# Kernel optimization log

Measured on AMD Instinct MI355X. Metric: run time of the kernel, lower is better.

## Reference

```python
import jax, jax.numpy as jnp
import numpy as np

N_NODE = 50000
N_EDGE = 625000
FDIM = 128
HID = 128
EPS = 1e-5


def setup_inputs() -> dict:
    key = jax.random.key(0)
    ks = jax.random.split(key, 12)
    node_feature = jax.random.normal(ks[0], (N_NODE, FDIM), dtype=jnp.float32)
    edge_matrix = jax.random.randint(ks[1], (2, N_EDGE), 0, N_NODE, dtype=jnp.int32)
    edge_feature = jax.random.normal(ks[2], (N_EDGE, FDIM), dtype=jnp.float32)
    in_dim = FDIM + FDIM  # concat(node, aggregated edge)
    s1 = 1.0 / np.sqrt(in_dim)
    s2 = 1.0 / np.sqrt(HID)
    W1 = jax.random.uniform(ks[3], (in_dim, HID), jnp.float32, -s1, s1)
    b1 = jax.random.uniform(ks[4], (HID,), jnp.float32, -s1, s1)
    W2 = jax.random.uniform(ks[5], (HID, HID), jnp.float32, -s2, s2)
    b2 = jax.random.uniform(ks[6], (HID,), jnp.float32, -s2, s2)
    W3 = jax.random.uniform(ks[7], (HID, FDIM), jnp.float32, -s2, s2)
    b3 = jax.random.uniform(ks[8], (FDIM,), jnp.float32, -s2, s2)
    gamma = jnp.ones((FDIM,), jnp.float32)
    beta = jnp.zeros((FDIM,), jnp.float32)
    return {"node_feature": node_feature, "edge_matrix": edge_matrix,
            "edge_feature": edge_feature, "W1": W1, "b1": b1, "W2": W2,
            "b2": b2, "W3": W3, "b3": b3, "gamma": gamma, "beta": beta}


def reference(node_feature, edge_matrix, edge_feature, W1, b1, W2, b2, W3, b3, gamma, beta):
    # receiver_idx = edge_matrix.T[:, 1] with edge_matrix [2, N_edge] -> row 1
    receiver_idx = edge_matrix[1]
    # scatter_add over receiver: [N_node, fdim]
    agg = jax.ops.segment_sum(edge_feature, receiver_idx, num_segments=node_feature.shape[0])
    x = jnp.concatenate([node_feature, agg], axis=-1)  # [N_node, 2*fdim]
    h = jax.nn.relu(x @ W1 + b1)
    h = jax.nn.relu(h @ W2 + b2)
    h = h @ W3 + b3
    # LayerNorm over last dim (eps = 1e-5, torch default)
    mu = jnp.mean(h, axis=-1, keepdims=True)
    var = jnp.mean((h - mu) ** 2, axis=-1, keepdims=True)
    h = (h - mu) * jax.lax.rsqrt(var + EPS) * gamma + beta
    return h + node_feature
```

## Files before the change

kernel.cpp:

```cpp
#include <hip/hip_runtime.h>
#include <hip/hip_bf16.h>

#define N_NODE 50000
#define N_EDGE 625000
#define FDIM 128
#define NB_SCAN 196

typedef __bf16 bf16x8 __attribute__((ext_vector_type(8)));
typedef float floatx4 __attribute__((ext_vector_type(4)));

#define MT 64
#define XS_LD 264
#define W_LD 40
#define H_LD 136

__global__ __launch_bounds__(256) void hist_kernel(
    const int* __restrict__ recv, int* __restrict__ count, int* __restrict__ pos)
{
    int e = blockIdx.x * 256 + threadIdx.x;
    if (e < N_EDGE) pos[e] = atomicAdd(&count[recv[e]], 1);
}

__global__ __launch_bounds__(256) void scan1_kernel(
    const int* __restrict__ count, int* __restrict__ off, int* __restrict__ bsum)
{
    __shared__ int s[256];
    int t = threadIdx.x;
    int i = blockIdx.x * 256 + t;
    int v = (i < N_NODE) ? count[i] : 0;
    s[t] = v;
    __syncthreads();
    for (int d = 1; d < 256; d <<= 1) {
        int x = (t >= d) ? s[t - d] : 0;
        __syncthreads();
        s[t] += x;
        __syncthreads();
    }
    if (i < N_NODE) off[i] = s[t] - v;
    if (t == 255) bsum[blockIdx.x] = s[255];
}

__global__ __launch_bounds__(256) void scan2_kernel(
    int* __restrict__ off, const int* __restrict__ bsum)
{
    __shared__ int s[256];
    int t = threadIdx.x;
    int v = (t < NB_SCAN) ? bsum[t] : 0;
    s[t] = v;
    __syncthreads();
    for (int d = 1; d < 256; d <<= 1) {
        int x = (t >= d) ? s[t - d] : 0;
        __syncthreads();
        s[t] += x;
        __syncthreads();
    }
    int i = blockIdx.x * 256 + t;
    if (i < N_NODE) off[i] += s[blockIdx.x] - ((blockIdx.x < NB_SCAN) ? bsum[blockIdx.x] : 0);
    if (i == N_NODE) off[i] = N_EDGE;
}

__global__ __launch_bounds__(256) void fill_kernel(
    const int* __restrict__ recv, const int* __restrict__ pos,
    const int* __restrict__ off, int* __restrict__ eid)
{
    int e = blockIdx.x * 256 + threadIdx.x;
    if (e < N_EDGE) {
        int r = recv[e];
        eid[off[r] + pos[e]] = e;
    }
}

__global__ __launch_bounds__(256) void gather_kernel(
    const float2* __restrict__ ef2, const int* __restrict__ off,
    const int* __restrict__ eid, int* __restrict__ agg32)
{
    int wave = threadIdx.x >> 6;
    int lane = threadIdx.x & 63;
    int node = blockIdx.x * 4 + wave;
    float ax = 0.f, ay = 0.f;
    int s0 = off[node], e0 = off[node + 1];
    for (int base = s0; base < e0; base += 64) {
        int cnt = e0 - base; if (cnt > 64) cnt = 64;
        int my_e = (lane < cnt) ? eid[base + lane] : 0;
        int j = 0;
        for (; j + 4 <= cnt; j += 4) {
            int ea = __shfl(my_e, j);
            int eb = __shfl(my_e, j + 1);
            int ec = __shfl(my_e, j + 2);
            int ed = __shfl(my_e, j + 3);
            float2 va = ef2[(long)ea * 64 + lane];
            float2 vb = ef2[(long)eb * 64 + lane];
            float2 vc = ef2[(long)ec * 64 + lane];
            float2 vd = ef2[(long)ed * 64 + lane];
            ax += va.x + vb.x + vc.x + vd.x;
            ay += va.y + vb.y + vc.y + vd.y;
        }
        for (; j < cnt; ++j) {
            int e = __shfl(my_e, j);
            float2 v = ef2[(long)e * 64 + lane];
            ax += v.x; ay += v.y;
        }
    }
    union { __bf16 b[2]; int iv; } u;
    u.b[0] = (__bf16)ax; u.b[1] = (__bf16)ay;
    agg32[(long)node * 64 + lane] = u.iv;
}

__global__ __launch_bounds__(256, 2) void mlp_kernel(
    const float* __restrict__ nodef, const int* __restrict__ agg32,
    const float* __restrict__ W1, const float* __restrict__ b1,
    const float* __restrict__ W2, const float* __restrict__ b2,
    const float* __restrict__ W3, const float* __restrict__ b3,
    const float* __restrict__ gamma, const float* __restrict__ beta,
    float* __restrict__ out)
{
    __shared__ __bf16 xs[MT * XS_LD];
    __shared__ __bf16 wb[128 * W_LD];
    __shared__ __bf16 h1[MT * H_LD];
    __bf16* h2 = xs;

    const int t = threadIdx.x;
    const int wave = t >> 6;
    const int lane = t & 63;
    const int quad = lane >> 4;
    const int l16 = lane & 15;
    const int w16 = wave << 4;
    const int q8 = quad << 3;
    const int node0 = blockIdx.x * MT;

    const float4* nf4 = (const float4*)nodef;
#pragma unroll
    for (int i = 0; i < 8; ++i) {
        int it = i * 256 + t;
        int row = it >> 5;
        int c4 = it & 31;
        int node = node0 + row;
        if (node >= N_NODE) node = N_NODE - 1;
        float4 v = nf4[(long)node * 32 + c4];
        union { __bf16 b[4]; short4 s; } u;
        u.b[0] = (__bf16)v.x; u.b[1] = (__bf16)v.y;
        u.b[2] = (__bf16)v.z; u.b[3] = (__bf16)v.w;
        *(short4*)&xs[row * XS_LD + c4 * 4] = u.s;
    }
    const int4* ag4 = (const int4*)agg32;
#pragma unroll
    for (int i = 0; i < 4; ++i) {
        int it = i * 256 + t;
        int row = it >> 4;
        int c8 = it & 15;
        int node = node0 + row;
        if (node >= N_NODE) node = N_NODE - 1;
        int4 v = ag4[(long)node * 16 + c8];
        *(int4*)&xs[row * XS_LD + 128 + c8 * 8] = v;
    }

    floatx4 acc[8];
    const floatx4 zero = {0.f, 0.f, 0.f, 0.f};

    auto stage_w = [&](const float* __restrict__ Wsrc, int k0) {
#pragma unroll
        for (int p = 0; p < 8; ++p) {
            int kl = p * 4 + ((t >> 7) << 1);
            int n = t & 127;
            float a0 = Wsrc[(k0 + kl) * 128 + n];
            float a1 = Wsrc[(k0 + kl + 1) * 128 + n];
            union { __bf16 b[2]; int i; } u;
            u.b[0] = (__bf16)a0; u.b[1] = (__bf16)a1;
            *(int*)&wb[n * W_LD + kl] = u.i;
        }
    };

    auto run_gemm = [&](const __bf16* A, int ldA, const float* __restrict__ Wsrc, int nk) {
#pragma unroll
        for (int nt = 0; nt < 8; ++nt) acc[nt] = zero;
        for (int kc = 0; kc < nk; ++kc) {
            stage_w(Wsrc, kc * 32);
            __syncthreads();
            bf16x8 a = *(const bf16x8*)&A[(w16 + l16) * ldA + kc * 32 + q8];
#pragma unroll
            for (int nt = 0; nt < 8; ++nt) {
                bf16x8 b = *(const bf16x8*)&wb[(nt * 16 + l16) * W_LD + q8];
                acc[nt] = __builtin_amdgcn_mfma_f32_16x16x32_bf16(a, b, acc[nt], 0, 0, 0);
            }
            __syncthreads();
        }
    };

    auto epilogue_relu = [&](const float* __restrict__ bias, __bf16* H) {
#pragma unroll
        for (int nt = 0; nt < 8; ++nt) {
            int col = nt * 16 + l16;
            float bv = bias[col];
#pragma unroll
            for (int r = 0; r < 4; ++r) {
                float v = acc[nt][r] + bv;
                v = v > 0.f ? v : 0.f;
                H[(w16 + quad * 4 + r) * H_LD + col] = (__bf16)v;
            }
        }
    };

    run_gemm(xs, XS_LD, W1, 8);
    epilogue_relu(b1, h1);
    run_gemm(h1, H_LD, W2, 4);
    epilogue_relu(b2, h2);
    run_gemm(h2, H_LD, W3, 4);

    float vout[8][4];
    float sum[4] = {0.f, 0.f, 0.f, 0.f};
    float sq[4]  = {0.f, 0.f, 0.f, 0.f};
#pragma unroll
    for (int nt = 0; nt < 8; ++nt) {
        int col = nt * 16 + l16;
        float bv = b3[col];
#pragma unroll
        for (int r = 0; r < 4; ++r) {
            float v = acc[nt][r] + bv;
            vout[nt][r] = v;
            sum[r] += v;
            sq[r] += v * v;
        }
    }
#pragma unroll
    for (int r = 0; r < 4; ++r) {
#pragma unroll
        for (int offs = 1; offs < 16; offs <<= 1) {
            sum[r] += __shfl_xor(sum[r], offs);
            sq[r]  += __shfl_xor(sq[r], offs);
        }
    }
    float mu[4], rs[4];
#pragma unroll
    for (int r = 0; r < 4; ++r) {
        mu[r] = sum[r] * (1.f / 128.f);
        float var = sq[r] * (1.f / 128.f) - mu[r] * mu[r];
        rs[r] = rsqrtf(var + 1e-5f);
    }
#pragma unroll
    for (int nt = 0; nt < 8; ++nt) {
        int col = nt * 16 + l16;
        float g = gamma[col], be = beta[col];
#pragma unroll
        for (int r = 0; r < 4; ++r) {
            int row = w16 + quad * 4 + r;
            int node = node0 + row;
            if (node < N_NODE) {
                long o = (long)node * 128 + col;
                out[o] = (vout[nt][r] - mu[r]) * rs[r] * g + be + nodef[o];
            }
        }
    }
}

extern "C" void kernel_launch(void* const* d_in, const int* in_sizes, int n_in,
                              void* d_out, int out_size, void* d_ws, size_t ws_size,
                              hipStream_t stream)
{
    const float* nodef = (const float*)d_in[0];
    const int*   em    = (const int*)d_in[1];
    const float* ef    = (const float*)d_in[2];
    const float* W1    = (const float*)d_in[3];
    const float* b1    = (const float*)d_in[4];
    const float* W2    = (const float*)d_in[5];
    const float* b2    = (const float*)d_in[6];
    const float* W3    = (const float*)d_in[7];
    const float* b3    = (const float*)d_in[8];
    const float* gamma = (const float*)d_in[9];
    const float* beta  = (const float*)d_in[10];
    float* out = (float*)d_out;

    int* count = (int*)d_ws;
    int* pos   = count + 50048;
    int* off   = pos + 625024;
    int* bsum  = off + 50048;
    int* eid   = bsum + 256;
    int* agg32 = eid + 625024;

    const int* recv = em + N_EDGE;

    hipMemsetAsync(count, 0, (size_t)N_NODE * sizeof(int), stream);

    int eblocks = (N_EDGE + 255) / 256;
    hist_kernel<<<eblocks, 256, 0, stream>>>(recv, count, pos);
    scan1_kernel<<<NB_SCAN, 256, 0, stream>>>(count, off, bsum);
    scan2_kernel<<<NB_SCAN, 256, 0, stream>>>(off, bsum);
    fill_kernel<<<eblocks, 256, 0, stream>>>(recv, pos, off, eid);
    gather_kernel<<<N_NODE / 4, 256, 0, stream>>>((const float2*)ef, off, eid, agg32);

    int mblocks = (N_NODE + MT - 1) / MT;
    mlp_kernel<<<mblocks, 256, 0, stream>>>(nodef, agg32, W1, b1, W2, b2,
                                            W3, b3, gamma, beta, out);
}
```

Measured before the change: 553.6 us.

## Prepack weights into MFMA fragments and widen gather to float4 half-wave loads

A new kernel converts W1/W2/W3 once per call into bf16 MFMA B-fragment order, so the MLP kernel loads B operands straight from global memory into registers. This removes the per-k-chunk LDS staging and its two barriers per chunk, and it prefetches the next k-chunk's A and B fragments. The gather kernel now splits each wave into two halves that each read a full 512B edge row with float4 loads, then combines the halves with a shuffle. Launch bounds rise to 3 blocks per CU, and the LDS weight buffer is dropped. The cost is more register pressure and repeated global/L2 reads of the weights from every block.

```diff
diff --git a/kernel.cpp b/kernel.cpp
--- a/kernel.cpp
+++ b/kernel.cpp
@@ -11,8 +11,11 @@
 
 #define MT 64
 #define XS_LD 264
-#define W_LD 40
 #define H_LD 136
+
+__device__ inline bf16x8 as_bf16x8(uint4 v) {
+    union { uint4 u; bf16x8 b; } c; c.u = v; return c.b;
+}
 
 __global__ __launch_bounds__(256) void hist_kernel(
     const int* __restrict__ recv, int* __restrict__ count, int* __restrict__ pos)
@@ -70,52 +73,84 @@
     }
 }
 
+__global__ __launch_bounds__(256) void wrepack_kernel(
+    const float* __restrict__ W1, const float* __restrict__ W2,
+    const float* __restrict__ W3, uint4* __restrict__ wp)
+{
+    int g = blockIdx.x * 256 + threadIdx.x;
+    int lane = g & 63;
+    int nt = (g >> 6) & 7;
+    int tile = g >> 9;
+    const float* W; int k0;
+    if (tile < 8)       { W = W1; k0 = tile * 32; }
+    else if (tile < 12) { W = W2; k0 = (tile - 8) * 32; }
+    else                { W = W3; k0 = (tile - 12) * 32; }
+    int n = nt * 16 + (lane & 15);
+    int kb = k0 + (lane >> 4) * 8;
+    union { __bf16 b[8]; uint4 u; } p;
+#pragma unroll
+    for (int j = 0; j < 8; ++j) p.b[j] = (__bf16)W[(kb + j) * 128 + n];
+    wp[g] = p.u;
+}
+
 __global__ __launch_bounds__(256) void gather_kernel(
-    const float2* __restrict__ ef2, const int* __restrict__ off,
-    const int* __restrict__ eid, int* __restrict__ agg32)
+    const float4* __restrict__ ef4, const int* __restrict__ off,
+    const int* __restrict__ eid, uint2* __restrict__ agg)
 {
     int wave = threadIdx.x >> 6;
     int lane = threadIdx.x & 63;
     int node = blockIdx.x * 4 + wave;
-    float ax = 0.f, ay = 0.f;
+    int half = lane >> 5;
+    int c = lane & 31;
+    float4 acc = {0.f, 0.f, 0.f, 0.f};
     int s0 = off[node], e0 = off[node + 1];
     for (int base = s0; base < e0; base += 64) {
         int cnt = e0 - base; if (cnt > 64) cnt = 64;
-        int my_e = (lane < cnt) ? eid[base + lane] : 0;
+        int ids = (lane < cnt) ? eid[base + lane] : 0;
         int j = 0;
-        for (; j + 4 <= cnt; j += 4) {
-            int ea = __shfl(my_e, j);
-            int eb = __shfl(my_e, j + 1);
-            int ec = __shfl(my_e, j + 2);
-            int ed = __shfl(my_e, j + 3);
-            float2 va = ef2[(long)ea * 64 + lane];
-            float2 vb = ef2[(long)eb * 64 + lane];
-            float2 vc = ef2[(long)ec * 64 + lane];
-            float2 vd = ef2[(long)ed * 64 + lane];
-            ax += va.x + vb.x + vc.x + vd.x;
-            ay += va.y + vb.y + vc.y + vd.y;
-        }
-        for (; j < cnt; ++j) {
-            int e = __shfl(my_e, j);
-            float2 v = ef2[(long)e * 64 + lane];
-            ax += v.x; ay += v.y;
-        }
-    }
-    union { __bf16 b[2]; int iv; } u;
-    u.b[0] = (__bf16)ax; u.b[1] = (__bf16)ay;
-    agg32[(long)node * 64 + lane] = u.iv;
-}
-
-__global__ __launch_bounds__(256, 2) void mlp_kernel(
+        for (; j + 8 <= cnt; j += 8) {
+            int ea = __shfl(ids, j + half);
+            int eb = __shfl(ids, j + 2 + half);
+            int ec = __shfl(ids, j + 4 + half);
+            int ed = __shfl(ids, j + 6 + half);
+            float4 va = ef4[(long)ea * 32 + c];
+            float4 vb = ef4[(long)eb * 32 + c];
+            float4 vc = ef4[(long)ec * 32 + c];
+            float4 vd = ef4[(long)ed * 32 + c];
+            acc.x += va.x + vb.x + vc.x + vd.x;
+            acc.y += va.y + vb.y + vc.y + vd.y;
+            acc.z += va.z + vb.z + vc.z + vd.z;
+            acc.w += va.w + vb.w + vc.w + vd.w;
+        }
+        for (; j < cnt; j += 2) {
+            if (j + half < cnt) {
+                int e = __shfl(ids, j + half);
+                float4 v = ef4[(long)e * 32 + c];
+                acc.x += v.x; acc.y += v.y; acc.z += v.z; acc.w += v.w;
+            }
+        }
+    }
+    acc.x += __shfl_xor(acc.x, 32);
+    acc.y += __shfl_xor(acc.y, 32);
+    acc.z += __shfl_xor(acc.z, 32);
+    acc.w += __shfl_xor(acc.w, 32);
+    if (half == 0) {
+        union { __bf16 b[4]; uint2 u; } p;
+        p.b[0] = (__bf16)acc.x; p.b[1] = (__bf16)acc.y;
+        p.b[2] = (__bf16)acc.z; p.b[3] = (__bf16)acc.w;
+        agg[(long)node * 32 + c] = p.u;
+    }
+}
+
+__global__ __launch_bounds__(256, 3) void mlp_kernel(
     const float* __restrict__ nodef, const int* __restrict__ agg32,
-    const float* __restrict__ W1, const float* __restrict__ b1,
-    const float* __restrict__ W2, const float* __restrict__ b2,
-    const float* __restrict__ W3, const float* __restrict__ b3,
+    const uint4* __restrict__ wp,
+    const float* __restrict__ b1, const float* __restrict__ b2,
+    const float* __restrict__ b3,
     const float* __restrict__ gamma, const float* __restrict__ beta,
     float* __restrict__ out)
 {
     __shared__ __bf16 xs[MT * XS_LD];
-    __shared__ __bf16 wb[128 * W_LD];
     __shared__ __bf16 h1[MT * H_LD];
     __bf16* h2 = xs;
 
@@ -157,32 +192,28 @@
     floatx4 acc[8];
     const floatx4 zero = {0.f, 0.f, 0.f, 0.f};
 
-    auto stage_w = [&](const float* __restrict__ Wsrc, int k0) {
-#pragma unroll
-        for (int p = 0; p < 8; ++p) {
-            int kl = p * 4 + ((t >> 7) << 1);
-            int n = t & 127;
-            float a0 = Wsrc[(k0 + kl) * 128 + n];
-            float a1 = Wsrc[(k0 + kl + 1) * 128 + n];
-            union { __bf16 b[2]; int i; } u;
-            u.b[0] = (__bf16)a0; u.b[1] = (__bf16)a1;
-            *(int*)&wb[n * W_LD + kl] = u.i;
-        }
-    };
-
-    auto run_gemm = [&](const __bf16* A, int ldA, const float* __restrict__ Wsrc, int nk) {
+    auto run_gemm = [&](const __bf16* A, int ldA, const uint4* __restrict__ wpt, int nk) {
 #pragma unroll
         for (int nt = 0; nt < 8; ++nt) acc[nt] = zero;
+        const __bf16* arow = A + (w16 + l16) * ldA + q8;
+        bf16x8 a = *(const bf16x8*)arow;
+        bf16x8 b[8];
+#pragma unroll
+        for (int nt = 0; nt < 8; ++nt) b[nt] = as_bf16x8(wpt[nt * 64 + lane]);
         for (int kc = 0; kc < nk; ++kc) {
-            stage_w(Wsrc, kc * 32);
-            __syncthreads();
-            bf16x8 a = *(const bf16x8*)&A[(w16 + l16) * ldA + kc * 32 + q8];
-#pragma unroll
-            for (int nt = 0; nt < 8; ++nt) {
-                bf16x8 b = *(const bf16x8*)&wb[(nt * 16 + l16) * W_LD + q8];
-                acc[nt] = __builtin_amdgcn_mfma_f32_16x16x32_bf16(a, b, acc[nt], 0, 0, 0);
+            bf16x8 a2; bf16x8 b2[8];
+            if (kc + 1 < nk) {
+                a2 = *(const bf16x8*)(arow + (kc + 1) * 32);
+#pragma unroll
+                for (int nt = 0; nt < 8; ++nt)
+                    b2[nt] = as_bf16x8(wpt[((kc + 1) * 8 + nt) * 64 + lane]);
             }
-            __syncthreads();
+#pragma unroll
+            for (int nt = 0; nt < 8; ++nt)
+                acc[nt] = __builtin_amdgcn_mfma_f32_16x16x32_bf16(a, b[nt], acc[nt], 0, 0, 0);
+            a = a2;
+#pragma unroll
+            for (int nt = 0; nt < 8; ++nt) b[nt] = b2[nt];
         }
     };
 
@@ -200,11 +231,14 @@
         }
     };
 
-    run_gemm(xs, XS_LD, W1, 8);
+    __syncthreads();
+    run_gemm(xs, XS_LD, wp, 8);
     epilogue_relu(b1, h1);
-    run_gemm(h1, H_LD, W2, 4);
+    __syncthreads();
+    run_gemm(h1, H_LD, wp + 8 * 8 * 64, 4);
     epilogue_relu(b2, h2);
-    run_gemm(h2, H_LD, W3, 4);
+    __syncthreads();
+    run_gemm(h2, H_LD, wp + 12 * 8 * 64, 4);
 
     float vout[8][4];
     float sum[4] = {0.f, 0.f, 0.f, 0.f};
@@ -275,19 +309,22 @@
     int* bsum  = off + 50048;
     int* eid   = bsum + 256;
     int* agg32 = eid + 625024;
+    uint4* wp  = (uint4*)(agg32 + 3200000);
 
     const int* recv = em + N_EDGE;
 
     hipMemsetAsync(count, 0, (size_t)N_NODE * sizeof(int), stream);
+
+    wrepack_kernel<<<32, 256, 0, stream>>>(W1, W2, W3, wp);
 
     int eblocks = (N_EDGE + 255) / 256;
     hist_kernel<<<eblocks, 256, 0, stream>>>(recv, count, pos);
     scan1_kernel<<<NB_SCAN, 256, 0, stream>>>(count, off, bsum);
     scan2_kernel<<<NB_SCAN, 256, 0, stream>>>(off, bsum);
     fill_kernel<<<eblocks, 256, 0, stream>>>(recv, pos, off, eid);
-    gather_kernel<<<N_NODE / 4, 256, 0, stream>>>((const float2*)ef, off, eid, agg32);
+    gather_kernel<<<N_NODE / 4, 256, 0, stream>>>((const float4*)ef, off, eid, (uint2*)agg32);
 
     int mblocks = (N_NODE + MT - 1) / MT;
-    mlp_kernel<<<mblocks, 256, 0, stream>>>(nodef, agg32, W1, b1, W2, b2,
-                                            W3, b3, gamma, beta, out);
-}
+    mlp_kernel<<<mblocks, 256, 0, stream>>>(nodef, agg32, wp, b1, b2, b3,
+                                            gamma, beta, out);
+}
```

Result: no change. 548.0 us (-1.0%).
